# Kernel tuning notes

Measured on AMD Instinct MI355X. Metric: run time of the kernel, lower is better.

Reference implementation:

```python
import jax, jax.numpy as jnp
import numpy as np

WS = 32          # window_size -> N = WS*WS = 1024
DIM = 1024
HEADS = 16
BATCH = 16


def _local_mask():
    # token i maps to grid cell (i//WS, i%WS); attend iff within 3x3 neighborhood
    idx = jnp.arange(WS * WS)
    r, c = idx // WS, idx % WS
    return (jnp.abs(r[:, None] - r[None, :]) <= 1) & (jnp.abs(c[:, None] - c[None, :]) <= 1)


def setup_inputs() -> dict:
    key = jax.random.key(0)
    k1, k2, k3 = jax.random.split(key, 3)
    N = WS * WS
    x = jax.random.normal(k1, (BATCH, N, DIM), dtype=jnp.float32)
    w_qkv = jax.random.normal(k2, (3 * DIM, DIM), dtype=jnp.float32) * 0.02
    w_proj = jax.random.normal(k3, (DIM, DIM), dtype=jnp.float32) * 0.02
    b_proj = jnp.zeros((DIM,), dtype=jnp.float32)
    return {"x": x, "w_qkv": w_qkv, "w_proj": w_proj, "b_proj": b_proj}


def reference(x, w_qkv, w_proj, b_proj):
    B, N, C = x.shape
    H = HEADS
    D = C // H
    scale = D ** (-0.5)
    # qkv projection: torch Linear is x @ W^T
    qkv = (x @ w_qkv.T).reshape(B, N, 3, H, D).transpose(2, 0, 3, 1, 4)  # (3,B,H,N,D)
    q, k, v = qkv[0], qkv[1], qkv[2]
    attn = jnp.einsum('bhnd,bhmd->bhnm', q, k) * scale  # (B,H,N,N)
    mask = _local_mask()  # (N,N) bool
    attn = jnp.where(mask[None, None], attn, -jnp.inf)
    attn = jax.nn.softmax(attn, axis=-1)
    out = jnp.einsum('bhnm,bhmd->bhnd', attn, v)          # (B,H,N,D)
    out = out.transpose(0, 2, 1, 3).reshape(B, N, C)      # (B,N,C)
    return out @ w_proj.T + b_proj
```

## Files before the change

### kernel.cpp

```cpp
#include <hip/hip_runtime.h>
#include <hip/hip_bf16.h>
#include <stdint.h>


typedef __bf16 bf16;
typedef __bf16 bf16x4_t __attribute__((ext_vector_type(4)));
typedef __bf16 bf16x8_t __attribute__((ext_vector_type(8)));
typedef float f32x4_t __attribute__((ext_vector_type(4)));

static __device__ __forceinline__ void gload_lds16(const void* g, void* l) {
  __builtin_amdgcn_global_load_lds((__attribute__((address_space(1))) void*)g,
                                   (__attribute__((address_space(3))) void*)l,
                                   16, 0, 0);
}

static __device__ __forceinline__ void block_barrier() {
  asm volatile("" ::: "memory");
  __builtin_amdgcn_s_barrier();
  asm volatile("" ::: "memory");
}

__global__ void cvt_all(const float* __restrict__ x, const float* __restrict__ wq,
                        const float* __restrict__ wp, bf16* __restrict__ xb,
                        bf16* __restrict__ wqb, bf16* __restrict__ wpb) {
  constexpr int NX = 4194304, NWQ = 786432;
  int i = blockIdx.x * blockDim.x + threadIdx.x;
  const float* src; bf16* dst; int off;
  if (i < NX)            { src = x;  dst = xb;  off = i; }
  else if (i < NX + NWQ) { src = wq; dst = wqb; off = i - NX; }
  else                   { src = wp; dst = wpb; off = i - (NX + NWQ); }
  float4 v = reinterpret_cast<const float4*>(src)[off];
  bf16x4_t o;
  o[0] = (bf16)v.x; o[1] = (bf16)v.y; o[2] = (bf16)v.z; o[3] = (bf16)v.w;
  reinterpret_cast<bf16x4_t*>(dst)[off] = o;
}

template<int OUT_BF16, int MWF>
__global__ __launch_bounds__(512, 2)
void gemm_bk32(const bf16* __restrict__ A, const bf16* __restrict__ Bm,
               void* __restrict__ Cout, const float* __restrict__ bias,
               int M, int N, int K) {
  constexpr int BM      = MWF * 32;
  constexpr int A_BYTES = BM * 64;
  constexpr int SLOT    = A_BYTES + 16384;
  constexpr int ALOADS  = MWF / 4;
  constexpr int LPT     = ALOADS + 2;
  extern __shared__ __align__(16) char lds[];

  const int tid = threadIdx.x;
  const int w = tid >> 6, lane = tid & 63;
  const int fr = lane & 15, g = lane >> 4;
  const int wr = w >> 2, wc = w & 3;

  const int nwg = gridDim.x * gridDim.y;
  int lid = blockIdx.y * gridDim.x + blockIdx.x;
  lid = (lid & 7) * (nwg >> 3) + (lid >> 3);
  const int bx = lid % gridDim.x, by = lid / gridDim.x;
  const int row0 = by * BM, col0 = bx * 256;

  const bf16* Ag = A + (size_t)row0 * K;
  const bf16* Bg = Bm + (size_t)col0 * K;
  const int srow = tid >> 2;
  const int scol = ((tid & 3) ^ ((tid >> 3) & 3)) * 8;
  const int nkt  = K >> 5;

  f32x4_t acc[MWF][4] = {};

  auto stage = [&](int kt, int slot) {
    const int kb = kt << 5;
    char* sb = lds + slot * SLOT;
#pragma unroll
    for (int n = 0; n < ALOADS; ++n)
      gload_lds16(Ag + (size_t)(n * 128 + srow) * K + kb + scol,
                  sb + n * 8192 + tid * 16);
#pragma unroll
    for (int n = 0; n < 2; ++n)
      gload_lds16(Bg + (size_t)(n * 128 + srow) * K + kb + scol,
                  sb + A_BYTES + n * 8192 + tid * 16);
  };

  const int uxor = ((fr >> 1) & 3) << 4;

  stage(0, 0);
  stage(1, 1);
  if constexpr (LPT == 4) asm volatile("s_waitcnt vmcnt(4)" ::: "memory");
  else                    asm volatile("s_waitcnt vmcnt(3)" ::: "memory");
  block_barrier();

  for (int kt = 0; kt < nkt; ++kt) {
    const char* cA = lds + (kt & 1) * SLOT;
    const char* cB = cA + A_BYTES;
    const bool pf = (kt + 2 < nkt);

    bf16x8_t a0[MWF / 2], a1[MWF / 2], b0[2], b1[2];

    auto lda = [&](bf16x8_t (&dst)[MWF / 2], int q) {
#pragma unroll
      for (int i = 0; i < MWF / 2; ++i) {
        const int row = wr * (MWF * 16) + (q * (MWF / 2) + i) * 16 + fr;
        dst[i] = *reinterpret_cast<const bf16x8_t*>(cA + (row << 6) + ((g << 4) ^ uxor));
      }
    };
    auto ldb = [&](bf16x8_t (&dst)[2], int q) {
#pragma unroll
      for (int j = 0; j < 2; ++j) {
        const int row = wc * 64 + (q * 2 + j) * 16 + fr;
        dst[j] = *reinterpret_cast<const bf16x8_t*>(cB + (row << 6) + ((g << 4) ^ uxor));
      }
    };

    lda(a0, 0);
    ldb(b0, 0);
#pragma unroll
    for (int i = 0; i < MWF / 2; ++i)
#pragma unroll
      for (int j = 0; j < 2; ++j)
        acc[i][j] = __builtin_amdgcn_mfma_f32_16x16x32_bf16(a0[i], b0[j], acc[i][j], 0, 0, 0);
    ldb(b1, 1);
#pragma unroll
    for (int i = 0; i < MWF / 2; ++i)
#pragma unroll
      for (int j = 0; j < 2; ++j)
        acc[i][2 + j] = __builtin_amdgcn_mfma_f32_16x16x32_bf16(a0[i], b1[j], acc[i][2 + j], 0, 0, 0);
    lda(a1, 1);
#pragma unroll
    for (int i = 0; i < MWF / 2; ++i)
#pragma unroll
      for (int j = 0; j < 2; ++j)
        acc[MWF / 2 + i][2 + j] = __builtin_amdgcn_mfma_f32_16x16x32_bf16(
            a1[i], b1[j], acc[MWF / 2 + i][2 + j], 0, 0, 0);
#pragma unroll
    for (int i = 0; i < MWF / 2; ++i)
#pragma unroll
      for (int j = 0; j < 2; ++j)
        acc[MWF / 2 + i][j] = __builtin_amdgcn_mfma_f32_16x16x32_bf16(
            a1[i], b0[j], acc[MWF / 2 + i][j], 0, 0, 0);

    block_barrier();
    if (pf) stage(kt + 2, kt & 1);
    if (kt < nkt - 2) {
      if constexpr (LPT == 4) asm volatile("s_waitcnt vmcnt(4)" ::: "memory");
      else                    asm volatile("s_waitcnt vmcnt(3)" ::: "memory");
    } else {
      asm volatile("s_waitcnt vmcnt(0)" ::: "memory");
    }
    block_barrier();
  }

#pragma unroll
  for (int fm = 0; fm < MWF; ++fm) {
    const int rbase = row0 + wr * (MWF * 16) + fm * 16 + g * 4;
#pragma unroll
    for (int fn = 0; fn < 4; ++fn) {
      const int col = col0 + wc * 64 + fn * 16 + fr;
#pragma unroll
      for (int r = 0; r < 4; ++r) {
        const size_t idx = (size_t)(rbase + r) * N + col;
        if constexpr (OUT_BF16) {
          reinterpret_cast<bf16*>(Cout)[idx] = (bf16)acc[fm][fn][r];
        } else {
          reinterpret_cast<float*>(Cout)[idx] = acc[fm][fn][r] + bias[col];
        }
      }
    }
  }
}

__global__ __launch_bounds__(256)
void local_attn(const bf16* __restrict__ qkv, bf16* __restrict__ outp) {
  const int tid  = threadIdx.x;
  const int wave = tid >> 6, lane = tid & 63;
  const int tsub = lane >> 3, ch = lane & 7;
  const int gt = (blockIdx.x * 4 + wave) * 8 + tsub;
  const int i  = gt & 1023;
  const int bh = gt >> 10;
  const int h  = bh & 15, b = bh >> 4;
  const int r  = i >> 5, c = i & 31;

  const bf16* base = qkv + (size_t)(b * 1024) * 3072 + h * 64 + ch * 8;

  bf16x8_t qv = *reinterpret_cast<const bf16x8_t*>(base + (size_t)i * 3072);
  float qf[8];
#pragma unroll
  for (int e = 0; e < 8; ++e) qf[e] = (float)qv[e];

  float s[9];
  bool valid[9];
#pragma unroll
  for (int dr = -1; dr <= 1; ++dr) {
#pragma unroll
    for (int dc = -1; dc <= 1; ++dc) {
      const int idx = (dr + 1) * 3 + (dc + 1);
      const int rr = r + dr, cc = c + dc;
      valid[idx] = (rr >= 0 && rr < 32 && cc >= 0 && cc < 32);
      float sv = -1e30f;
      if (valid[idx]) {
        const int j = rr * 32 + cc;
        bf16x8_t kv = *reinterpret_cast<const bf16x8_t*>(base + (size_t)j * 3072 + 1024);
        float ps = 0.f;
#pragma unroll
        for (int e = 0; e < 8; ++e) ps += qf[e] * (float)kv[e];
        ps += __shfl_xor(ps, 1);
        ps += __shfl_xor(ps, 2);
        ps += __shfl_xor(ps, 4);
        sv = ps * 0.125f;
      }
      s[idx] = sv;
    }
  }

  float mx = s[0];
#pragma unroll
  for (int t = 1; t < 9; ++t) mx = fmaxf(mx, s[t]);

  float p[9], denom = 0.f;
#pragma unroll
  for (int t = 0; t < 9; ++t) {
    p[t] = valid[t] ? __expf(s[t] - mx) : 0.f;
    denom += p[t];
  }

  float o[8] = {};
#pragma unroll
  for (int dr = -1; dr <= 1; ++dr) {
#pragma unroll
    for (int dc = -1; dc <= 1; ++dc) {
      const int idx = (dr + 1) * 3 + (dc + 1);
      if (valid[idx]) {
        const int j = (r + dr) * 32 + (c + dc);
        bf16x8_t vv = *reinterpret_cast<const bf16x8_t*>(base + (size_t)j * 3072 + 2048);
        const float pw = p[idx];
#pragma unroll
        for (int e = 0; e < 8; ++e) o[e] += pw * (float)vv[e];
      }
    }
  }

  const float inv = 1.f / denom;
  bf16x8_t ov;
#pragma unroll
  for (int e = 0; e < 8; ++e) ov[e] = (bf16)(o[e] * inv);
  *reinterpret_cast<bf16x8_t*>(outp + (size_t)(b * 1024 + i) * 1024 + h * 64 + ch * 8) = ov;
}

extern "C" void kernel_launch(void* const* d_in, const int* in_sizes, int n_in,
                              void* d_out, int out_size, void* d_ws, size_t ws_size,
                              hipStream_t stream) {
  const float* x      = (const float*)d_in[0];
  const float* w_qkv  = (const float*)d_in[1];
  const float* w_proj = (const float*)d_in[2];
  const float* b_proj = (const float*)d_in[3];
  float* out = (float*)d_out;

  const size_t nx   = (size_t)16384 * 1024;
  const size_t nwq  = (size_t)3072 * 1024;
  const size_t nwp  = (size_t)1024 * 1024;
  const size_t nqkv = (size_t)16384 * 3072;

  bf16* x_bf  = (bf16*)d_ws;
  bf16* wq_bf = x_bf + nx;
  bf16* wp_bf = wq_bf + nwq;
  bf16* qkv   = wp_bf + nwp;
  bf16* attn  = qkv + nqkv;

  (void)hipFuncSetAttribute((const void*)&gemm_bk32<1, 8>,
                            hipFuncAttributeMaxDynamicSharedMemorySize, 65536);
  (void)hipFuncSetAttribute((const void*)&gemm_bk32<0, 4>,
                            hipFuncAttributeMaxDynamicSharedMemorySize, 49152);

  cvt_all<<<20480, 256, 0, stream>>>(x, w_qkv, w_proj, x_bf, wq_bf, wp_bf);

  gemm_bk32<1, 8><<<dim3(3072 / 256, 16384 / 256), 512, 65536, stream>>>(
      x_bf, wq_bf, qkv, nullptr, 16384, 3072, 1024);

  local_attn<<<8192, 256, 0, stream>>>(qkv, attn);

  gemm_bk32<0, 4><<<dim3(1024 / 256, 16384 / 128), 512, 49152, stream>>>(
      attn, wp_bf, out, b_proj, 16384, 1024, 1024);
}
```

Baseline: 220.5 us.

## Load GEMM B operand directly from global into registers, stage only A in LDS

Both GEMMs now stop staging the weight (B) tile through shared memory. Each wave loads its own B fragments straight from global memory into registers, double-buffered one k-step ahead, while A is still double-buffered in LDS through global_load_lds. This cuts LDS footprint and LDS read traffic for B, and switches to static shared memory. The cost is that each B element is read from global/L2 by multiple waves (wr rows) rather than once per block, and global-load latency is exposed directly to the MFMA loop.

```diff
diff --git a/kernel.cpp b/kernel.cpp
--- a/kernel.cpp
+++ b/kernel.cpp
@@ -37,15 +37,13 @@
 
 template<int OUT_BF16, int MWF>
 __global__ __launch_bounds__(512, 2)
-void gemm_bk32(const bf16* __restrict__ A, const bf16* __restrict__ Bm,
+void gemm_breg(const bf16* __restrict__ A, const bf16* __restrict__ Bm,
                void* __restrict__ Cout, const float* __restrict__ bias,
                int M, int N, int K) {
   constexpr int BM      = MWF * 32;
   constexpr int A_BYTES = BM * 64;
-  constexpr int SLOT    = A_BYTES + 16384;
   constexpr int ALOADS  = MWF / 4;
-  constexpr int LPT     = ALOADS + 2;
-  extern __shared__ __align__(16) char lds[];
+  __shared__ __align__(16) char lds[2 * A_BYTES];
 
   const int tid = threadIdx.x;
   const int w = tid >> 6, lane = tid & 63;
@@ -59,92 +57,68 @@
   const int row0 = by * BM, col0 = bx * 256;
 
   const bf16* Ag = A + (size_t)row0 * K;
-  const bf16* Bg = Bm + (size_t)col0 * K;
   const int srow = tid >> 2;
   const int scol = ((tid & 3) ^ ((tid >> 3) & 3)) * 8;
   const int nkt  = K >> 5;
 
+  const bf16* Bl = Bm + (size_t)(col0 + wc * 64 + fr) * K + g * 8;
+
   f32x4_t acc[MWF][4] = {};
 
-  auto stage = [&](int kt, int slot) {
+  auto stageA = [&](int kt, int slot) {
     const int kb = kt << 5;
-    char* sb = lds + slot * SLOT;
+    char* sb = lds + slot * A_BYTES;
 #pragma unroll
     for (int n = 0; n < ALOADS; ++n)
       gload_lds16(Ag + (size_t)(n * 128 + srow) * K + kb + scol,
                   sb + n * 8192 + tid * 16);
-#pragma unroll
-    for (int n = 0; n < 2; ++n)
-      gload_lds16(Bg + (size_t)(n * 128 + srow) * K + kb + scol,
-                  sb + A_BYTES + n * 8192 + tid * 16);
   };
+  auto loadB = [&](bf16x8_t (&bv)[4], int kt) {
+    const int kb = kt << 5;
+#pragma unroll
+    for (int j = 0; j < 4; ++j)
+      bv[j] = *reinterpret_cast<const bf16x8_t*>(Bl + (size_t)(j * 16) * K + kb);
+  };
 
   const int uxor = ((fr >> 1) & 3) << 4;
 
-  stage(0, 0);
-  stage(1, 1);
-  if constexpr (LPT == 4) asm volatile("s_waitcnt vmcnt(4)" ::: "memory");
-  else                    asm volatile("s_waitcnt vmcnt(3)" ::: "memory");
-  block_barrier();
-
-  for (int kt = 0; kt < nkt; ++kt) {
-    const char* cA = lds + (kt & 1) * SLOT;
-    const char* cB = cA + A_BYTES;
-    const bool pf = (kt + 2 < nkt);
-
-    bf16x8_t a0[MWF / 2], a1[MWF / 2], b0[2], b1[2];
-
-    auto lda = [&](bf16x8_t (&dst)[MWF / 2], int q) {
-#pragma unroll
-      for (int i = 0; i < MWF / 2; ++i) {
-        const int row = wr * (MWF * 16) + (q * (MWF / 2) + i) * 16 + fr;
-        dst[i] = *reinterpret_cast<const bf16x8_t*>(cA + (row << 6) + ((g << 4) ^ uxor));
-      }
-    };
-    auto ldb = [&](bf16x8_t (&dst)[2], int q) {
-#pragma unroll
-      for (int j = 0; j < 2; ++j) {
-        const int row = wc * 64 + (q * 2 + j) * 16 + fr;
-        dst[j] = *reinterpret_cast<const bf16x8_t*>(cB + (row << 6) + ((g << 4) ^ uxor));
-      }
-    };
-
-    lda(a0, 0);
-    ldb(b0, 0);
-#pragma unroll
-    for (int i = 0; i < MWF / 2; ++i)
-#pragma unroll
-      for (int j = 0; j < 2; ++j)
-        acc[i][j] = __builtin_amdgcn_mfma_f32_16x16x32_bf16(a0[i], b0[j], acc[i][j], 0, 0, 0);
-    ldb(b1, 1);
-#pragma unroll
-    for (int i = 0; i < MWF / 2; ++i)
-#pragma unroll
-      for (int j = 0; j < 2; ++j)
-        acc[i][2 + j] = __builtin_amdgcn_mfma_f32_16x16x32_bf16(a0[i], b1[j], acc[i][2 + j], 0, 0, 0);
-    lda(a1, 1);
-#pragma unroll
-    for (int i = 0; i < MWF / 2; ++i)
-#pragma unroll
-      for (int j = 0; j < 2; ++j)
-        acc[MWF / 2 + i][2 + j] = __builtin_amdgcn_mfma_f32_16x16x32_bf16(
-            a1[i], b1[j], acc[MWF / 2 + i][2 + j], 0, 0, 0);
-#pragma unroll
-    for (int i = 0; i < MWF / 2; ++i)
-#pragma unroll
-      for (int j = 0; j < 2; ++j)
-        acc[MWF / 2 + i][j] = __builtin_amdgcn_mfma_f32_16x16x32_bf16(
-            a1[i], b0[j], acc[MWF / 2 + i][j], 0, 0, 0);
-
+  auto body = [&](int kt, const bf16x8_t (&bv)[4], bf16x8_t (&bnxt)[4],
+                  bool pfB, bool pfA) {
+    if (pfB) loadB(bnxt, kt + 1);
+    const char* cA = lds + (kt & 1) * A_BYTES;
+    bf16x8_t a[MWF];
+#pragma unroll
+    for (int i = 0; i < MWF; ++i) {
+      const int row = wr * (MWF * 16) + i * 16 + fr;
+      a[i] = *reinterpret_cast<const bf16x8_t*>(cA + (row << 6) + ((g << 4) ^ uxor));
+    }
+#pragma unroll
+    for (int i = 0; i < MWF; ++i)
+#pragma unroll
+      for (int j = 0; j < 4; ++j)
+        acc[i][j] = __builtin_amdgcn_mfma_f32_16x16x32_bf16(a[i], bv[j], acc[i][j], 0, 0, 0);
     block_barrier();
-    if (pf) stage(kt + 2, kt & 1);
-    if (kt < nkt - 2) {
-      if constexpr (LPT == 4) asm volatile("s_waitcnt vmcnt(4)" ::: "memory");
-      else                    asm volatile("s_waitcnt vmcnt(3)" ::: "memory");
+    if (pfA) {
+      stageA(kt + 2, kt & 1);
+      if constexpr (ALOADS == 2) asm volatile("s_waitcnt vmcnt(2)" ::: "memory");
+      else                       asm volatile("s_waitcnt vmcnt(1)" ::: "memory");
     } else {
       asm volatile("s_waitcnt vmcnt(0)" ::: "memory");
     }
     block_barrier();
+  };
+
+  stageA(0, 0);
+  stageA(1, 1);
+  bf16x8_t bA_[4], bB_[4];
+  loadB(bA_, 0);
+  if constexpr (ALOADS == 2) asm volatile("s_waitcnt vmcnt(2)" ::: "memory");
+  else                       asm volatile("s_waitcnt vmcnt(1)" ::: "memory");
+  block_barrier();
+
+  for (int kt = 0; kt < nkt; kt += 2) {
+    body(kt,     bA_, bB_, kt + 1 < nkt, kt + 2 < nkt);
+    body(kt + 1, bB_, bA_, kt + 2 < nkt, kt + 3 < nkt);
   }
 
 #pragma unroll
@@ -263,18 +237,13 @@
   bf16* qkv   = wp_bf + nwp;
   bf16* attn  = qkv + nqkv;
 
-  (void)hipFuncSetAttribute((const void*)&gemm_bk32<1, 8>,
-                            hipFuncAttributeMaxDynamicSharedMemorySize, 65536);
-  (void)hipFuncSetAttribute((const void*)&gemm_bk32<0, 4>,
-                            hipFuncAttributeMaxDynamicSharedMemorySize, 49152);
-
   cvt_all<<<20480, 256, 0, stream>>>(x, w_qkv, w_proj, x_bf, wq_bf, wp_bf);
 
-  gemm_bk32<1, 8><<<dim3(3072 / 256, 16384 / 256), 512, 65536, stream>>>(
+  gemm_breg<1, 8><<<dim3(3072 / 256, 16384 / 256), 512, 0, stream>>>(
       x_bf, wq_bf, qkv, nullptr, 16384, 3072, 1024);
 
   local_attn<<<8192, 256, 0, stream>>>(qkv, attn);
 
-  gemm_bk32<0, 4><<<dim3(1024 / 256, 16384 / 128), 512, 49152, stream>>>(
+  gemm_breg<0, 4><<<dim3(1024 / 256, 16384 / 128), 512, 0, stream>>>(
       attn, wp_bf, out, b_proj, 16384, 1024, 1024);
 }
```

Measured after the change: 315.1 us. +42.9%, slower.

## Use triple-buffered LDS pipeline in GEMMs and batch neighbor loads in local attention

Applied to the files above, without the earlier changes.

The GEMM moves from a double-buffered LDS scheme with two barriers per k-step to a three-slot ring. Each iteration issues the prefetch for tile k+2 before computing tile k, then waits and hits a single barrier. The output projection GEMM now uses 256x256 tiles instead of 128x256. The attention kernel clamps neighbor indices and applies an additive mask, so all 18 K/V loads are issued up front without branches, trading more registers and redundant loads at borders for higher memory-level parallelism. The triple buffer needs 96KB of LDS per block, which may limit how many blocks fit per CU compared with the declared launch bounds.

```diff
diff --git a/kernel.cpp b/kernel.cpp
--- a/kernel.cpp
+++ b/kernel.cpp
@@ -35,16 +35,12 @@
   reinterpret_cast<bf16x4_t*>(dst)[off] = o;
 }
 
-template<int OUT_BF16, int MWF>
+template<int OUT_BF16>
 __global__ __launch_bounds__(512, 2)
-void gemm_bk32(const bf16* __restrict__ A, const bf16* __restrict__ Bm,
-               void* __restrict__ Cout, const float* __restrict__ bias,
-               int M, int N, int K) {
-  constexpr int BM      = MWF * 32;
-  constexpr int A_BYTES = BM * 64;
-  constexpr int SLOT    = A_BYTES + 16384;
-  constexpr int ALOADS  = MWF / 4;
-  constexpr int LPT     = ALOADS + 2;
+void gemm3s(const bf16* __restrict__ A, const bf16* __restrict__ Bm,
+            void* __restrict__ Cout, const float* __restrict__ bias,
+            int M, int N, int K) {
+  constexpr int SLOT = 32768;
   extern __shared__ __align__(16) char lds[];
 
   const int tid = threadIdx.x;
@@ -56,7 +52,7 @@
   int lid = blockIdx.y * gridDim.x + blockIdx.x;
   lid = (lid & 7) * (nwg >> 3) + (lid >> 3);
   const int bx = lid % gridDim.x, by = lid / gridDim.x;
-  const int row0 = by * BM, col0 = bx * 256;
+  const int row0 = by * 256, col0 = bx * 256;
 
   const bf16* Ag = A + (size_t)row0 * K;
   const bf16* Bg = Bm + (size_t)col0 * K;
@@ -64,40 +60,37 @@
   const int scol = ((tid & 3) ^ ((tid >> 3) & 3)) * 8;
   const int nkt  = K >> 5;
 
-  f32x4_t acc[MWF][4] = {};
+  f32x4_t acc[8][4] = {};
 
   auto stage = [&](int kt, int slot) {
     const int kb = kt << 5;
     char* sb = lds + slot * SLOT;
-#pragma unroll
-    for (int n = 0; n < ALOADS; ++n)
-      gload_lds16(Ag + (size_t)(n * 128 + srow) * K + kb + scol,
-                  sb + n * 8192 + tid * 16);
-#pragma unroll
-    for (int n = 0; n < 2; ++n)
-      gload_lds16(Bg + (size_t)(n * 128 + srow) * K + kb + scol,
-                  sb + A_BYTES + n * 8192 + tid * 16);
+    gload_lds16(Ag + (size_t)(srow) * K + kb + scol,       sb + tid * 16);
+    gload_lds16(Ag + (size_t)(128 + srow) * K + kb + scol, sb + 8192 + tid * 16);
+    gload_lds16(Bg + (size_t)(srow) * K + kb + scol,       sb + 16384 + tid * 16);
+    gload_lds16(Bg + (size_t)(128 + srow) * K + kb + scol, sb + 24576 + tid * 16);
   };
 
   const int uxor = ((fr >> 1) & 3) << 4;
 
   stage(0, 0);
   stage(1, 1);
-  if constexpr (LPT == 4) asm volatile("s_waitcnt vmcnt(4)" ::: "memory");
-  else                    asm volatile("s_waitcnt vmcnt(3)" ::: "memory");
+  asm volatile("s_waitcnt vmcnt(4)" ::: "memory");
   block_barrier();
 
+  int sl = 0;
   for (int kt = 0; kt < nkt; ++kt) {
-    const char* cA = lds + (kt & 1) * SLOT;
-    const char* cB = cA + A_BYTES;
     const bool pf = (kt + 2 < nkt);
-
-    bf16x8_t a0[MWF / 2], a1[MWF / 2], b0[2], b1[2];
-
-    auto lda = [&](bf16x8_t (&dst)[MWF / 2], int q) {
-#pragma unroll
-      for (int i = 0; i < MWF / 2; ++i) {
-        const int row = wr * (MWF * 16) + (q * (MWF / 2) + i) * 16 + fr;
+    int s2 = sl + 2; if (s2 >= 3) s2 -= 3;
+    if (pf) stage(kt + 2, s2);
+    const char* cA = lds + sl * SLOT;
+    const char* cB = cA + 16384;
+
+    bf16x8_t a0[4], a1[4], b0[2], b1[2];
+    auto lda = [&](bf16x8_t (&dst)[4], int q) {
+#pragma unroll
+      for (int i = 0; i < 4; ++i) {
+        const int row = wr * 128 + (q * 4 + i) * 16 + fr;
         dst[i] = *reinterpret_cast<const bf16x8_t*>(cA + (row << 6) + ((g << 4) ^ uxor));
       }
     };
@@ -112,44 +105,39 @@
     lda(a0, 0);
     ldb(b0, 0);
 #pragma unroll
-    for (int i = 0; i < MWF / 2; ++i)
+    for (int i = 0; i < 4; ++i)
 #pragma unroll
       for (int j = 0; j < 2; ++j)
         acc[i][j] = __builtin_amdgcn_mfma_f32_16x16x32_bf16(a0[i], b0[j], acc[i][j], 0, 0, 0);
     ldb(b1, 1);
 #pragma unroll
-    for (int i = 0; i < MWF / 2; ++i)
+    for (int i = 0; i < 4; ++i)
 #pragma unroll
       for (int j = 0; j < 2; ++j)
         acc[i][2 + j] = __builtin_amdgcn_mfma_f32_16x16x32_bf16(a0[i], b1[j], acc[i][2 + j], 0, 0, 0);
     lda(a1, 1);
 #pragma unroll
-    for (int i = 0; i < MWF / 2; ++i)
-#pragma unroll
-      for (int j = 0; j < 2; ++j)
-        acc[MWF / 2 + i][2 + j] = __builtin_amdgcn_mfma_f32_16x16x32_bf16(
-            a1[i], b1[j], acc[MWF / 2 + i][2 + j], 0, 0, 0);
-#pragma unroll
-    for (int i = 0; i < MWF / 2; ++i)
-#pragma unroll
-      for (int j = 0; j < 2; ++j)
-        acc[MWF / 2 + i][j] = __builtin_amdgcn_mfma_f32_16x16x32_bf16(
-            a1[i], b0[j], acc[MWF / 2 + i][j], 0, 0, 0);
-
+    for (int i = 0; i < 4; ++i)
+#pragma unroll
+      for (int j = 0; j < 2; ++j)
+        acc[4 + i][2 + j] = __builtin_amdgcn_mfma_f32_16x16x32_bf16(
+            a1[i], b1[j], acc[4 + i][2 + j], 0, 0, 0);
+#pragma unroll
+    for (int i = 0; i < 4; ++i)
+#pragma unroll
+      for (int j = 0; j < 2; ++j)
+        acc[4 + i][j] = __builtin_amdgcn_mfma_f32_16x16x32_bf16(
+            a1[i], b0[j], acc[4 + i][j], 0, 0, 0);
+
+    if (pf) asm volatile("s_waitcnt vmcnt(4)" ::: "memory");
+    else    asm volatile("s_waitcnt vmcnt(0)" ::: "memory");
     block_barrier();
-    if (pf) stage(kt + 2, kt & 1);
-    if (kt < nkt - 2) {
-      if constexpr (LPT == 4) asm volatile("s_waitcnt vmcnt(4)" ::: "memory");
-      else                    asm volatile("s_waitcnt vmcnt(3)" ::: "memory");
-    } else {
-      asm volatile("s_waitcnt vmcnt(0)" ::: "memory");
-    }
-    block_barrier();
-  }
-
-#pragma unroll
-  for (int fm = 0; fm < MWF; ++fm) {
-    const int rbase = row0 + wr * (MWF * 16) + fm * 16 + g * 4;
+    sl = (sl + 1 == 3) ? 0 : sl + 1;
+  }
+
+#pragma unroll
+  for (int fm = 0; fm < 8; ++fm) {
+    const int rbase = row0 + wr * 128 + fm * 16 + g * 4;
 #pragma unroll
     for (int fn = 0; fn < 4; ++fn) {
       const int col = col0 + wc * 64 + fn * 16 + fr;
@@ -184,56 +172,47 @@
 #pragma unroll
   for (int e = 0; e < 8; ++e) qf[e] = (float)qv[e];
 
+  int jj[9]; float inval[9];
+#pragma unroll
+  for (int t = 0; t < 9; ++t) {
+    const int dr = t / 3 - 1, dc = t % 3 - 1;
+    const int rr = r + dr, cc = c + dc;
+    const int rcl = min(max(rr, 0), 31), ccl = min(max(cc, 0), 31);
+    jj[t] = rcl * 32 + ccl;
+    inval[t] = (rr == rcl && cc == ccl) ? 0.f : -1e30f;
+  }
+
+  bf16x8_t kv[9], vv[9];
+#pragma unroll
+  for (int t = 0; t < 9; ++t)
+    kv[t] = *reinterpret_cast<const bf16x8_t*>(base + (size_t)jj[t] * 3072 + 1024);
+#pragma unroll
+  for (int t = 0; t < 9; ++t)
+    vv[t] = *reinterpret_cast<const bf16x8_t*>(base + (size_t)jj[t] * 3072 + 2048);
+
   float s[9];
-  bool valid[9];
-#pragma unroll
-  for (int dr = -1; dr <= 1; ++dr) {
-#pragma unroll
-    for (int dc = -1; dc <= 1; ++dc) {
-      const int idx = (dr + 1) * 3 + (dc + 1);
-      const int rr = r + dr, cc = c + dc;
-      valid[idx] = (rr >= 0 && rr < 32 && cc >= 0 && cc < 32);
-      float sv = -1e30f;
-      if (valid[idx]) {
-        const int j = rr * 32 + cc;
-        bf16x8_t kv = *reinterpret_cast<const bf16x8_t*>(base + (size_t)j * 3072 + 1024);
-        float ps = 0.f;
-#pragma unroll
-        for (int e = 0; e < 8; ++e) ps += qf[e] * (float)kv[e];
-        ps += __shfl_xor(ps, 1);
-        ps += __shfl_xor(ps, 2);
-        ps += __shfl_xor(ps, 4);
-        sv = ps * 0.125f;
-      }
-      s[idx] = sv;
-    }
+#pragma unroll
+  for (int t = 0; t < 9; ++t) {
+    float ps = 0.f;
+#pragma unroll
+    for (int e = 0; e < 8; ++e) ps += qf[e] * (float)kv[t][e];
+    ps += __shfl_xor(ps, 1);
+    ps += __shfl_xor(ps, 2);
+    ps += __shfl_xor(ps, 4);
+    s[t] = ps * 0.125f + inval[t];
   }
 
   float mx = s[0];
 #pragma unroll
   for (int t = 1; t < 9; ++t) mx = fmaxf(mx, s[t]);
 
-  float p[9], denom = 0.f;
+  float denom = 0.f, o[8] = {};
 #pragma unroll
   for (int t = 0; t < 9; ++t) {
-    p[t] = valid[t] ? __expf(s[t] - mx) : 0.f;
-    denom += p[t];
-  }
-
-  float o[8] = {};
-#pragma unroll
-  for (int dr = -1; dr <= 1; ++dr) {
-#pragma unroll
-    for (int dc = -1; dc <= 1; ++dc) {
-      const int idx = (dr + 1) * 3 + (dc + 1);
-      if (valid[idx]) {
-        const int j = (r + dr) * 32 + (c + dc);
-        bf16x8_t vv = *reinterpret_cast<const bf16x8_t*>(base + (size_t)j * 3072 + 2048);
-        const float pw = p[idx];
-#pragma unroll
-        for (int e = 0; e < 8; ++e) o[e] += pw * (float)vv[e];
-      }
-    }
+    const float p = __expf(s[t] - mx);
+    denom += p;
+#pragma unroll
+    for (int e = 0; e < 8; ++e) o[e] += p * (float)vv[t][e];
   }
 
   const float inv = 1.f / denom;
@@ -263,18 +242,18 @@
   bf16* qkv   = wp_bf + nwp;
   bf16* attn  = qkv + nqkv;
 
-  (void)hipFuncSetAttribute((const void*)&gemm_bk32<1, 8>,
-                            hipFuncAttributeMaxDynamicSharedMemorySize, 65536);
-  (void)hipFuncSetAttribute((const void*)&gemm_bk32<0, 4>,
-                            hipFuncAttributeMaxDynamicSharedMemorySize, 49152);
+  (void)hipFuncSetAttribute((const void*)&gemm3s<1>,
+                            hipFuncAttributeMaxDynamicSharedMemorySize, 98304);
+  (void)hipFuncSetAttribute((const void*)&gemm3s<0>,
+                            hipFuncAttributeMaxDynamicSharedMemorySize, 98304);
 
   cvt_all<<<20480, 256, 0, stream>>>(x, w_qkv, w_proj, x_bf, wq_bf, wp_bf);
 
-  gemm_bk32<1, 8><<<dim3(3072 / 256, 16384 / 256), 512, 65536, stream>>>(
+  gemm3s<1><<<dim3(3072 / 256, 16384 / 256), 512, 98304, stream>>>(
       x_bf, wq_bf, qkv, nullptr, 16384, 3072, 1024);
 
   local_attn<<<8192, 256, 0, stream>>>(qkv, attn);
 
-  gemm_bk32<0, 4><<<dim3(1024 / 256, 16384 / 128), 512, 49152, stream>>>(
+  gemm3s<0><<<dim3(1024 / 256, 16384 / 256), 512, 98304, stream>>>(
       attn, wp_bf, out, b_proj, 16384, 1024, 1024);
 }
```

Measured after the change: 213.0 us. 3.4% less time.
